# Kernel tuning notes

Measured on AMD Instinct MI355X. Metric: run time of the kernel, lower is better.

The kernel has to match this reference:

```python
import jax, jax.numpy as jnp
import numpy as np
from functools import partial

NUM_STEPS = 30  # Euler integration steps (inte_steps)


def _point_sample(vol, pts):
    """Trilinear sample of vol [C,D,H,W] at pts [N,3] (voxel coords, (d,h,w) order).
    Matches torch grid_sample(mode='bilinear', padding_mode='border', align_corners=True)
    after the normalize+flip done in PointPooling. Returns [C,N]."""
    dims = jnp.asarray(vol.shape[1:], dtype=pts.dtype)  # (D,H,W)
    p = jnp.clip(pts, 0.0, dims - 1.0)  # border padding == clamp coords
    p0 = jnp.floor(p)
    frac = p - p0  # [N,3]
    i0 = p0.astype(jnp.int32)
    i1 = jnp.minimum(i0 + 1, (dims - 1.0).astype(jnp.int32))
    d0, h0, w0 = i0[:, 0], i0[:, 1], i0[:, 2]
    d1, h1, w1 = i1[:, 0], i1[:, 1], i1[:, 2]
    fd, fh, fw = frac[:, 0], frac[:, 1], frac[:, 2]
    g = lambda d, h, w: vol[:, d, h, w]  # [C,N] gather
    c000, c001 = g(d0, h0, w0), g(d0, h0, w1)
    c010, c011 = g(d0, h1, w0), g(d0, h1, w1)
    c100, c101 = g(d1, h0, w0), g(d1, h0, w1)
    c110, c111 = g(d1, h1, w0), g(d1, h1, w1)
    c00 = c000 * (1 - fw) + c001 * fw
    c01 = c010 * (1 - fw) + c011 * fw
    c10 = c100 * (1 - fw) + c101 * fw
    c11 = c110 * (1 - fw) + c111 * fw
    c0 = c00 * (1 - fh) + c01 * fh
    c1 = c10 * (1 - fh) + c11 * fh
    return c0 * (1 - fd) + c1 * fd  # [C,N]


def _interp(flow, x):
    # flow [B,3,D,H,W], x [B,N,3] -> [B,N,3]
    out = jax.vmap(_point_sample)(flow, x)  # [B,3,N]
    return jnp.transpose(out, (0, 2, 1))


def _integrate_euler(flow, x, num_steps):
    flow = flow * (1.0 / num_steps)
    def step(x, _):
        return x + _interp(flow, x), None
    x, _ = jax.lax.scan(step, x, None, length=num_steps)
    return x


def _forward(verts, affine, flow_field):
    B, N, _ = verts.shape
    ones = jnp.ones((B, N, 1), dtype=verts.dtype)
    homog = jnp.concatenate([verts, ones], axis=-1)  # [B,N,4]
    pred = jnp.einsum('bij,bnj->bni', affine, homog)[..., :3]
    aux = _integrate_euler(flow_field, pred, NUM_STEPS)
    flow_int = aux - pred  # [B,N,3]
    pred = aux
    flow_int = jnp.transpose(flow_int, (0, 2, 1))[..., None, None]  # [B,3,N,1,1]
    homog2 = jnp.concatenate([pred, ones], axis=-1)
    inv_aff = jnp.linalg.inv(affine)
    pred = jnp.einsum('bij,bnj->bni', inv_aff, homog2)[..., :3]
    return pred, flow_int


def setup_inputs() -> dict:
    key = jax.random.key(0)
    k1, k2, k3 = jax.random.split(key, 3)
    B, N = 2, 140000
    D = H = W = 192
    dims = jnp.asarray([D - 1, H - 1, W - 1], dtype=jnp.float32)
    verts = jax.random.uniform(k1, (B, N, 3), dtype=jnp.float32) * dims
    affine = jnp.eye(4, dtype=jnp.float32)[None] + 0.01 * jax.random.normal(k2, (B, 4, 4), dtype=jnp.float32)
    flow_field = jax.random.normal(k3, (B, 3, D, H, W), dtype=jnp.float32)
    return {"verts": verts, "affine": affine, "flow_field": flow_field}


def reference(verts, affine, flow_field):
    return _forward(verts, affine, flow_field)
```

## Files before the change

### kernel.cpp

```cpp
#include <hip/hip_runtime.h>

#define NSTEPS 30
#define DIM 192
static constexpr int DHW = DIM * DIM * DIM;

__global__ void invert4x4_kernel(const float* __restrict__ aff,
                                 float* __restrict__ out, int B) {
    int b = blockIdx.x * blockDim.x + threadIdx.x;
    if (b >= B) return;
    double m[4][8];
    for (int r = 0; r < 4; r++) {
        for (int c = 0; c < 4; c++) {
            m[r][c] = (double)aff[b * 16 + r * 4 + c];
            m[r][c + 4] = (r == c) ? 1.0 : 0.0;
        }
    }
    for (int col = 0; col < 4; col++) {
        int piv = col;
        double best = fabs(m[col][col]);
        for (int r = col + 1; r < 4; r++) {
            double a = fabs(m[r][col]);
            if (a > best) { best = a; piv = r; }
        }
        if (piv != col) {
            for (int c = 0; c < 8; c++) {
                double t = m[col][c]; m[col][c] = m[piv][c]; m[piv][c] = t;
            }
        }
        double inv = 1.0 / m[col][col];
        for (int c = 0; c < 8; c++) m[col][c] *= inv;
        for (int r = 0; r < 4; r++) {
            if (r == col) continue;
            double f = m[r][col];
            if (f != 0.0)
                for (int c = 0; c < 8; c++) m[r][c] -= f * m[col][c];
        }
    }
    for (int r = 0; r < 4; r++)
        for (int c = 0; c < 4; c++)
            out[b * 16 + r * 4 + c] = (float)m[r][c + 4];
}

__global__ __launch_bounds__(256) void deform_kernel(
    const float* __restrict__ verts,
    const float* __restrict__ affine,
    const float* __restrict__ flow,
    const float* __restrict__ invaff,
    float* __restrict__ out_pred,
    float* __restrict__ out_flow,
    int N, int B) {
    int idx = blockIdx.x * blockDim.x + threadIdx.x;
    if (idx >= B * N) return;
    int b = idx / N;
    int n = idx - b * N;

    const float* A = affine + b * 16;
    const float* v = verts + ((size_t)b * N + n) * 3;
    float vx = v[0], vy = v[1], vz = v[2];
    float x = A[0] * vx + A[1] * vy + A[2]  * vz + A[3];
    float y = A[4] * vx + A[5] * vy + A[6]  * vz + A[7];
    float z = A[8] * vx + A[9] * vy + A[10] * vz + A[11];
    const float px = x, py = y, pz = z;

    const float* F = flow + (size_t)b * 3 * DHW;
    const float scale = (float)(1.0 / NSTEPS);

    float cc[3][8];
    int key = -1;

    for (int s = 0; s < NSTEPS; s++) {
        float pd = fminf(fmaxf(x, 0.0f), (float)(DIM - 1));
        float ph = fminf(fmaxf(y, 0.0f), (float)(DIM - 1));
        float pw = fminf(fmaxf(z, 0.0f), (float)(DIM - 1));
        float fd0 = floorf(pd), fh0 = floorf(ph), fw0 = floorf(pw);
        int d0 = (int)fd0, h0 = (int)fh0, w0 = (int)fw0;
        float fd = pd - fd0, fh = ph - fh0, fw = pw - fw0;

        int k = (d0 * DIM + h0) * DIM + w0;
        if (k != key) {
            key = k;
            int d1 = min(d0 + 1, DIM - 1);
            int h1 = min(h0 + 1, DIM - 1);
            int w1 = min(w0 + 1, DIM - 1);
            int r00 = (d0 * DIM + h0) * DIM;
            int r01 = (d0 * DIM + h1) * DIM;
            int r10 = (d1 * DIM + h0) * DIM;
            int r11 = (d1 * DIM + h1) * DIM;
#pragma unroll
            for (int c = 0; c < 3; c++) {
                const float* Fc = F + (size_t)c * DHW;
                cc[c][0] = Fc[r00 + w0] * scale;
                cc[c][1] = Fc[r00 + w1] * scale;
                cc[c][2] = Fc[r01 + w0] * scale;
                cc[c][3] = Fc[r01 + w1] * scale;
                cc[c][4] = Fc[r10 + w0] * scale;
                cc[c][5] = Fc[r10 + w1] * scale;
                cc[c][6] = Fc[r11 + w0] * scale;
                cc[c][7] = Fc[r11 + w1] * scale;
            }
        }

        float omfw = 1.0f - fw, omfh = 1.0f - fh, omfd = 1.0f - fd;
        float vals[3];
#pragma unroll
        for (int c = 0; c < 3; c++) {
            float c00 = cc[c][0] * omfw + cc[c][1] * fw;
            float c01 = cc[c][2] * omfw + cc[c][3] * fw;
            float c10 = cc[c][4] * omfw + cc[c][5] * fw;
            float c11 = cc[c][6] * omfw + cc[c][7] * fw;
            float c0 = c00 * omfh + c01 * fh;
            float c1 = c10 * omfh + c11 * fh;
            vals[c] = c0 * omfd + c1 * fd;
        }
        x += vals[0];
        y += vals[1];
        z += vals[2];
    }

    float fx = x - px, fy = y - py, fz = z - pz;

    const float* Ai = invaff + b * 16;
    float ox = Ai[0] * x + Ai[1] * y + Ai[2]  * z + Ai[3];
    float oy = Ai[4] * x + Ai[5] * y + Ai[6]  * z + Ai[7];
    float oz = Ai[8] * x + Ai[9] * y + Ai[10] * z + Ai[11];

    size_t po = ((size_t)b * N + n) * 3;
    out_pred[po + 0] = ox;
    out_pred[po + 1] = oy;
    out_pred[po + 2] = oz;

    size_t fo = (size_t)b * 3 * N + n;
    out_flow[fo]         = fx;
    out_flow[fo + N]     = fy;
    out_flow[fo + 2 * N] = fz;
}

extern "C" void kernel_launch(void* const* d_in, const int* in_sizes, int n_in,
                              void* d_out, int out_size, void* d_ws, size_t ws_size,
                              hipStream_t stream) {
    const float* verts  = (const float*)d_in[0];
    const float* affine = (const float*)d_in[1];
    const float* flow   = (const float*)d_in[2];

    int B = in_sizes[1] / 16;
    int N = in_sizes[0] / (3 * B);

    float* invaff   = (float*)d_ws;
    float* out_pred = (float*)d_out;
    float* out_flow = out_pred + (size_t)B * N * 3;

    hipLaunchKernelGGL(invert4x4_kernel, dim3(1), dim3(64), 0, stream,
                       affine, invaff, B);

    int total = B * N;
    int block = 256;
    int grid = (total + block - 1) / block;
    hipLaunchKernelGGL(deform_kernel, dim3(grid), dim3(block), 0, stream,
                       verts, affine, flow, invaff, out_pred, out_flow, N, B);
}
```

Measured before the change: 331.3 us.

## Split each point's three flow channels across lanes and exchange via wave shuffles

Each point is now handled by three lanes, one per flow channel, with 21 points per 64-wide wave. Each lane gathers only its channel's 8 corners, and the three interpolated values are exchanged with __shfl so every lane advances the full position. This gives more parallelism for the latency-bound gathers and fewer registers per lane. In exchange it launches three times as many lanes, repeats the index math in each, adds three shuffles per step and leaves one lane per wave idle. The 4x4 inverse is also replaced with a closed-form cofactor formula, which drops partial pivoting.

```diff
diff --git a/kernel.cpp b/kernel.cpp
--- a/kernel.cpp
+++ b/kernel.cpp
@@ -3,42 +3,50 @@
 #define NSTEPS 30
 #define DIM 192
 static constexpr int DHW = DIM * DIM * DIM;
+static constexpr int PTS_PER_WAVE = 21;
 
 __global__ void invert4x4_kernel(const float* __restrict__ aff,
                                  float* __restrict__ out, int B) {
     int b = blockIdx.x * blockDim.x + threadIdx.x;
     if (b >= B) return;
-    double m[4][8];
-    for (int r = 0; r < 4; r++) {
-        for (int c = 0; c < 4; c++) {
-            m[r][c] = (double)aff[b * 16 + r * 4 + c];
-            m[r][c + 4] = (r == c) ? 1.0 : 0.0;
-        }
-    }
-    for (int col = 0; col < 4; col++) {
-        int piv = col;
-        double best = fabs(m[col][col]);
-        for (int r = col + 1; r < 4; r++) {
-            double a = fabs(m[r][col]);
-            if (a > best) { best = a; piv = r; }
-        }
-        if (piv != col) {
-            for (int c = 0; c < 8; c++) {
-                double t = m[col][c]; m[col][c] = m[piv][c]; m[piv][c] = t;
-            }
-        }
-        double inv = 1.0 / m[col][col];
-        for (int c = 0; c < 8; c++) m[col][c] *= inv;
-        for (int r = 0; r < 4; r++) {
-            if (r == col) continue;
-            double f = m[r][col];
-            if (f != 0.0)
-                for (int c = 0; c < 8; c++) m[r][c] -= f * m[col][c];
-        }
-    }
-    for (int r = 0; r < 4; r++)
-        for (int c = 0; c < 4; c++)
-            out[b * 16 + r * 4 + c] = (float)m[r][c + 4];
+    double a[16];
+#pragma unroll
+    for (int i = 0; i < 16; i++) a[i] = (double)aff[b * 16 + i];
+
+    double s0 = a[0]*a[5]  - a[4]*a[1];
+    double s1 = a[0]*a[6]  - a[4]*a[2];
+    double s2 = a[0]*a[7]  - a[4]*a[3];
+    double s3 = a[1]*a[6]  - a[5]*a[2];
+    double s4 = a[1]*a[7]  - a[5]*a[3];
+    double s5 = a[2]*a[7]  - a[6]*a[3];
+    double c5 = a[10]*a[15] - a[14]*a[11];
+    double c4 = a[9]*a[15]  - a[13]*a[11];
+    double c3 = a[9]*a[14]  - a[13]*a[10];
+    double c2 = a[8]*a[15]  - a[12]*a[11];
+    double c1 = a[8]*a[14]  - a[12]*a[10];
+    double c0 = a[8]*a[13]  - a[12]*a[9];
+    double det = s0*c5 - s1*c4 + s2*c3 + s3*c2 - s4*c1 + s5*c0;
+    double inv = 1.0 / det;
+
+    double o[16];
+    o[0]  = ( a[5]*c5 - a[6]*c4 + a[7]*c3) * inv;
+    o[1]  = (-a[1]*c5 + a[2]*c4 - a[3]*c3) * inv;
+    o[2]  = ( a[13]*s5 - a[14]*s4 + a[15]*s3) * inv;
+    o[3]  = (-a[9]*s5 + a[10]*s4 - a[11]*s3) * inv;
+    o[4]  = (-a[4]*c5 + a[6]*c2 - a[7]*c1) * inv;
+    o[5]  = ( a[0]*c5 - a[2]*c2 + a[3]*c1) * inv;
+    o[6]  = (-a[12]*s5 + a[14]*s2 - a[15]*s1) * inv;
+    o[7]  = ( a[8]*s5 - a[10]*s2 + a[11]*s1) * inv;
+    o[8]  = ( a[4]*c4 - a[5]*c2 + a[7]*c0) * inv;
+    o[9]  = (-a[0]*c4 + a[1]*c2 - a[3]*c0) * inv;
+    o[10] = ( a[12]*s4 - a[13]*s2 + a[15]*s0) * inv;
+    o[11] = (-a[8]*s4 + a[9]*s2 - a[11]*s0) * inv;
+    o[12] = (-a[4]*c3 + a[5]*c1 - a[6]*c0) * inv;
+    o[13] = ( a[0]*c3 - a[1]*c1 + a[2]*c0) * inv;
+    o[14] = (-a[12]*s3 + a[13]*s1 - a[14]*s0) * inv;
+    o[15] = ( a[8]*s3 - a[9]*s1 + a[10]*s0) * inv;
+#pragma unroll
+    for (int i = 0; i < 16; i++) out[b * 16 + i] = (float)o[i];
 }
 
 __global__ __launch_bounds__(256) void deform_kernel(
@@ -49,24 +57,35 @@
     float* __restrict__ out_pred,
     float* __restrict__ out_flow,
     int N, int B) {
-    int idx = blockIdx.x * blockDim.x + threadIdx.x;
-    if (idx >= B * N) return;
-    int b = idx / N;
-    int n = idx - b * N;
+    int lane = threadIdx.x & 63;
+    int wib  = threadIdx.x >> 6;
+    long gwave = (long)blockIdx.x * (blockDim.x >> 6) + wib;
+
+    int piw = lane / 3;
+    if (piw > PTS_PER_WAVE - 1) piw = PTS_PER_WAVE - 1;
+    int ch = lane - piw * 3;
+    if (ch > 2) ch = 2;
+
+    long pt = gwave * PTS_PER_WAVE + piw;
+    bool valid = (lane < 63) && (pt < (long)B * N);
+    long ptc = valid ? pt : ((long)B * N - 1);
+    int b = (int)(ptc / N);
+    int n = (int)(ptc - (long)b * N);
 
     const float* A = affine + b * 16;
-    const float* v = verts + ((size_t)b * N + n) * 3;
+    const float* v = verts + (size_t)ptc * 3;
     float vx = v[0], vy = v[1], vz = v[2];
     float x = A[0] * vx + A[1] * vy + A[2]  * vz + A[3];
     float y = A[4] * vx + A[5] * vy + A[6]  * vz + A[7];
     float z = A[8] * vx + A[9] * vy + A[10] * vz + A[11];
-    const float px = x, py = y, pz = z;
+    float p0 = (ch == 0) ? x : (ch == 1) ? y : z;
 
-    const float* F = flow + (size_t)b * 3 * DHW;
+    const float* Fc = flow + ((size_t)b * 3 + ch) * (size_t)DHW;
     const float scale = (float)(1.0 / NSTEPS);
 
-    float cc[3][8];
+    float cc[8];
     int key = -1;
+    int bl = piw * 3;
 
     for (int s = 0; s < NSTEPS; s++) {
         float pd = fminf(fmaxf(x, 0.0f), (float)(DIM - 1));
@@ -86,53 +105,39 @@
             int r01 = (d0 * DIM + h1) * DIM;
             int r10 = (d1 * DIM + h0) * DIM;
             int r11 = (d1 * DIM + h1) * DIM;
-#pragma unroll
-            for (int c = 0; c < 3; c++) {
-                const float* Fc = F + (size_t)c * DHW;
-                cc[c][0] = Fc[r00 + w0] * scale;
-                cc[c][1] = Fc[r00 + w1] * scale;
-                cc[c][2] = Fc[r01 + w0] * scale;
-                cc[c][3] = Fc[r01 + w1] * scale;
-                cc[c][4] = Fc[r10 + w0] * scale;
-                cc[c][5] = Fc[r10 + w1] * scale;
-                cc[c][6] = Fc[r11 + w0] * scale;
-                cc[c][7] = Fc[r11 + w1] * scale;
-            }
+            cc[0] = Fc[r00 + w0] * scale;
+            cc[1] = Fc[r00 + w1] * scale;
+            cc[2] = Fc[r01 + w0] * scale;
+            cc[3] = Fc[r01 + w1] * scale;
+            cc[4] = Fc[r10 + w0] * scale;
+            cc[5] = Fc[r10 + w1] * scale;
+            cc[6] = Fc[r11 + w0] * scale;
+            cc[7] = Fc[r11 + w1] * scale;
         }
 
         float omfw = 1.0f - fw, omfh = 1.0f - fh, omfd = 1.0f - fd;
-        float vals[3];
-#pragma unroll
-        for (int c = 0; c < 3; c++) {
-            float c00 = cc[c][0] * omfw + cc[c][1] * fw;
-            float c01 = cc[c][2] * omfw + cc[c][3] * fw;
-            float c10 = cc[c][4] * omfw + cc[c][5] * fw;
-            float c11 = cc[c][6] * omfw + cc[c][7] * fw;
-            float c0 = c00 * omfh + c01 * fh;
-            float c1 = c10 * omfh + c11 * fh;
-            vals[c] = c0 * omfd + c1 * fd;
-        }
-        x += vals[0];
-        y += vals[1];
-        z += vals[2];
+        float c00 = cc[0] * omfw + cc[1] * fw;
+        float c01 = cc[2] * omfw + cc[3] * fw;
+        float c10 = cc[4] * omfw + cc[5] * fw;
+        float c11 = cc[6] * omfw + cc[7] * fw;
+        float c0 = c00 * omfh + c01 * fh;
+        float c1 = c10 * omfh + c11 * fh;
+        float val = c0 * omfd + c1 * fd;
+
+        float v0 = __shfl(val, bl,     64);
+        float v1 = __shfl(val, bl + 1, 64);
+        float v2 = __shfl(val, bl + 2, 64);
+        x += v0; y += v1; z += v2;
     }
 
-    float fx = x - px, fy = y - py, fz = z - pz;
-
-    const float* Ai = invaff + b * 16;
-    float ox = Ai[0] * x + Ai[1] * y + Ai[2]  * z + Ai[3];
-    float oy = Ai[4] * x + Ai[5] * y + Ai[6]  * z + Ai[7];
-    float oz = Ai[8] * x + Ai[9] * y + Ai[10] * z + Ai[11];
-
-    size_t po = ((size_t)b * N + n) * 3;
-    out_pred[po + 0] = ox;
-    out_pred[po + 1] = oy;
-    out_pred[po + 2] = oz;
-
-    size_t fo = (size_t)b * 3 * N + n;
-    out_flow[fo]         = fx;
-    out_flow[fo + N]     = fy;
-    out_flow[fo + 2 * N] = fz;
+    if (valid) {
+        float posc = (ch == 0) ? x : (ch == 1) ? y : z;
+        float fint = posc - p0;
+        const float* Ai = invaff + b * 16 + ch * 4;
+        float o = Ai[0] * x + Ai[1] * y + Ai[2] * z + Ai[3];
+        out_pred[(size_t)ptc * 3 + ch] = o;
+        out_flow[(size_t)b * 3 * N + (size_t)ch * N + n] = fint;
+    }
 }
 
 extern "C" void kernel_launch(void* const* d_in, const int* in_sizes, int n_in,
@@ -152,9 +157,9 @@
     hipLaunchKernelGGL(invert4x4_kernel, dim3(1), dim3(64), 0, stream,
                        affine, invaff, B);
 
-    int total = B * N;
-    int block = 256;
-    int grid = (total + block - 1) / block;
-    hipLaunchKernelGGL(deform_kernel, dim3(grid), dim3(block), 0, stream,
+    long total_pts = (long)B * N;
+    long waves  = (total_pts + PTS_PER_WAVE - 1) / PTS_PER_WAVE;
+    long blocks = (waves + 3) / 4;
+    hipLaunchKernelGGL(deform_kernel, dim3((unsigned)blocks), dim3(256), 0, stream,
                        verts, affine, flow, invaff, out_pred, out_flow, N, B);
 }
```

Result: faster. 316.6 us (-4.4%).
